# Kernel tuning notes

Hardware: AMD Instinct MI355X
Metric: run time of the kernel (lower is better)

## Reference

```python
import jax, jax.numpy as jnp
import numpy as np

B, S, D, H = 4, 2048, 768, 12
DK = D // H

def setup_inputs() -> dict:
    key = jax.random.key(0)
    ks = jax.random.split(key, 9)
    s = 0.02
    return {
        "z": jax.random.normal(ks[0], (B, S, D), dtype=jnp.float32),
        "wq_w": jax.random.normal(ks[1], (D, D), dtype=jnp.float32) * s,
        "wq_b": jnp.zeros((D,), dtype=jnp.float32),
        "wk_w": jax.random.normal(ks[2], (D, D), dtype=jnp.float32) * s,
        "wk_b": jnp.zeros((D,), dtype=jnp.float32),
        "wv_w": jax.random.normal(ks[3], (D, D), dtype=jnp.float32) * s,
        "wv_b": jnp.zeros((D,), dtype=jnp.float32),
        "fc_w": jax.random.normal(ks[4], (D, D), dtype=jnp.float32) * s,
        "fc_b": jnp.zeros((D,), dtype=jnp.float32),
    }

def reference(z, wq_w, wq_b, wk_w, wk_b, wv_w, wv_b, fc_w, fc_b):
    # Dropout layers are treated as eval-mode (identity), as is standard for
    # a deterministic correctness baseline.
    b, s, d = z.shape
    temp = jnp.asarray(DK ** 0.5, dtype=z.dtype)
    # QKV projections -> [b, h, s, dk]
    def proj(w, bias):
        return (z @ w.T + bias).reshape(b, s, H, DK).transpose(0, 2, 1, 3)
    q = proj(wq_w, wq_b)
    k = proj(wk_w, wk_b)
    v = proj(wv_w, wv_b)
    # raw attention weights (pre-softmax), as returned by ScaleDotAttention
    attn_weights = jnp.einsum('bhqd,bhkd->bhqk', q / temp, k)  # [b,h,s,s]
    attn_probs = jax.nn.softmax(attn_weights, axis=-1)
    context = jnp.einsum('bhqk,bhkd->bhqd', attn_probs, v)  # [b,h,s,dk]
    avg_weights = jnp.sum(attn_weights, axis=1) / H  # [b,s,s]
    context = context.transpose(0, 2, 1, 3).reshape(b, s, d)
    attn_output = context @ fc_w.T + fc_b
    return attn_output, avg_weights
```

## Files before the change

### kernel.cpp

```cpp
#include <hip/hip_runtime.h>
#include <hip/hip_fp16.h>

#define Bc 4
#define Sc 2048
#define Dc 768
#define Hc 12
#define DKc 64

typedef _Float16 f16;
typedef __attribute__((ext_vector_type(8))) _Float16 f16x8;
typedef __attribute__((ext_vector_type(4))) _Float16 f16x4;
typedef __attribute__((ext_vector_type(4))) float f32x4;

static __device__ __forceinline__ f32x4 mfma16(f16x8 a, f16x8 b, f32x4 c) {
  return __builtin_amdgcn_mfma_f32_16x16x32_f16(a, b, c, 0, 0, 0);
}
static __device__ __forceinline__ f32x4 mfma16k16(f16x4 a, f16x4 b, f32x4 c) {
  return __builtin_amdgcn_mfma_f32_16x16x16f16(a, b, c, 0, 0, 0);
}

#define GLD16(g, l)                                              \
  __builtin_amdgcn_global_load_lds(                              \
      (const __attribute__((address_space(1))) void*)(g),        \
      (__attribute__((address_space(3))) void*)(l), 16, 0, 0)

#define SWZ(row, colB) (((row) << 7) + ((colB) ^ (((row) & 7) << 4)))

__global__ __launch_bounds__(256) void cvt5(
    const float* __restrict__ z, const float* __restrict__ w0,
    const float* __restrict__ w1, const float* __restrict__ w2,
    const float* __restrict__ w3, f16* __restrict__ oz, f16* __restrict__ o0,
    f16* __restrict__ o1, f16* __restrict__ o2, f16* __restrict__ o3) {
  const int bid = blockIdx.x;
  const float* in;
  f16* out;
  int i0;
  if (bid < 6144)      { in = z;  out = oz; i0 = bid * 256; }
  else if (bid < 6720) { in = w0; out = o0; i0 = (bid - 6144) * 256; }
  else if (bid < 7296) { in = w1; out = o1; i0 = (bid - 6720) * 256; }
  else if (bid < 7872) { in = w2; out = o2; i0 = (bid - 7296) * 256; }
  else                 { in = w3; out = o3; i0 = (bid - 7872) * 256; }
  const int i = i0 + threadIdx.x;
  float4 v = reinterpret_cast<const float4*>(in)[i];
  f16x4 o;
  o[0] = (f16)v.x; o[1] = (f16)v.y; o[2] = (f16)v.z; o[3] = (f16)v.w;
  reinterpret_cast<f16x4*>(out)[i] = o;
}

template <int MODE>
__global__ __launch_bounds__(512, 2) void gemm128x256(
    const f16* __restrict__ A0, const f16* __restrict__ W0,
    const f16* __restrict__ W1, const f16* __restrict__ W2,
    const float* __restrict__ bq, const float* __restrict__ bk,
    const float* __restrict__ bv, f16* __restrict__ Qb, f16* __restrict__ Kb,
    f16* __restrict__ Vt, float* __restrict__ avg) {
  constexpr int K = Dc;
  constexpr int NK = K / 32;
  const int tid = threadIdx.x;
  const int lane = tid & 63;
  const int w = tid >> 6;
  const int wr = w >> 2, wc = w & 3;
  const int l15 = lane & 15, lg = lane >> 4;

  const f16* Ab;
  const f16* Bb;
  long m0;
  int seg = 0, n0seg = 0, bat = 0, ncol0 = 0;
  if (MODE == 0) {
    const int wgid = (blockIdx.x & 7) * 72 + (blockIdx.x >> 3);
    const int mx = wgid / 9, nt = wgid % 9;
    m0 = (long)mx * 128;
    seg = nt / 3;
    n0seg = (nt % 3) * 256;
    const f16* Wsel = seg == 0 ? W0 : seg == 1 ? W1 : W2;
    Ab = A0 + m0 * K;
    Bb = Wsel + (long)n0seg * K;
  } else if (MODE == 1) {
    const int wgid = (blockIdx.x & 7) * 64 + (blockIdx.x >> 3);
    bat = wgid >> 7;
    const int t = wgid & 127;
    const int mx = t >> 3, nx = t & 7;
    m0 = (long)mx * 128;
    ncol0 = nx * 256;
    Ab = W0 + (long)bat * Sc * Dc + m0 * K;
    Bb = W1 + (long)bat * Sc * Dc + (long)ncol0 * K;
  } else {
    const int wgid = (blockIdx.x & 7) * 24 + (blockIdx.x >> 3);
    const int mx = wgid / 3, nx = wgid % 3;
    m0 = (long)mx * 128;
    ncol0 = nx * 256;
    Ab = A0 + m0 * K;
    Bb = W0 + (long)ncol0 * K;
  }

  __shared__ f16 As[2][128 * 32];
  __shared__ f16 Bs[2][256 * 32];

  const int lr = lane >> 2;
  const int lc = (lane & 3) * 8;
  const f16* Ag0 = Ab + (long)(w * 16 + lr) * K + lc;
  const f16* Bg0 = Bb + (long)(w * 32 + lr) * K + lc;
  const f16* Bg1 = Bg0 + (long)16 * K;

#define STG(buf, k0)                            \
  {                                             \
    GLD16(Ag0 + (k0), &As[buf][w * 512]);       \
    GLD16(Bg0 + (k0), &Bs[buf][w * 1024]);      \
    GLD16(Bg1 + (k0), &Bs[buf][w * 1024 + 512]);\
  }

  f32x4 acc[4][4] = {};

  STG(0, 0)
  STG(1, 32)

#pragma unroll 1
  for (int i = 0; i < NK; ++i) {
    if (i + 1 < NK) {
      asm volatile("s_waitcnt vmcnt(3)" ::: "memory");
    } else {
      asm volatile("s_waitcnt vmcnt(0)" ::: "memory");
    }
    __builtin_amdgcn_sched_barrier(0);
    __builtin_amdgcn_s_barrier();
    __builtin_amdgcn_sched_barrier(0);

    const f16* Asb = &As[i & 1][0];
    const f16* Bsb = &Bs[i & 1][0];
    f16x8 af[4], bf[4];
#pragma unroll
    for (int mi = 0; mi < 4; ++mi)
      af[mi] = *reinterpret_cast<const f16x8*>(
          &Asb[(wr * 64 + mi * 16 + l15) * 32 + lg * 8]);
#pragma unroll
    for (int ni = 0; ni < 4; ++ni)
      bf[ni] = *reinterpret_cast<const f16x8*>(
          &Bsb[(wc * 64 + ni * 16 + l15) * 32 + lg * 8]);
#pragma unroll
    for (int mi = 0; mi < 4; ++mi)
#pragma unroll
      for (int ni = 0; ni < 4; ++ni)
        acc[mi][ni] = mfma16(af[mi], bf[ni], acc[mi][ni]);

    __builtin_amdgcn_sched_barrier(0);
    __builtin_amdgcn_s_barrier();
    __builtin_amdgcn_sched_barrier(0);
    if (i + 2 < NK) STG(i & 1, (i + 2) * 32)
  }
#undef STG

  if (MODE == 0) {
    const float* bias = seg == 0 ? bq : seg == 1 ? bk : bv;
    float bvv[4];
#pragma unroll
    for (int ni = 0; ni < 4; ++ni)
      bvv[ni] = bias[n0seg + wc * 64 + ni * 16 + l15];
    if (seg < 2) {
      f16* dq = seg == 0 ? Qb : Kb;
#pragma unroll
      for (int mi = 0; mi < 4; ++mi) {
#pragma unroll
        for (int ni = 0; ni < 4; ++ni) {
          const long col = n0seg + wc * 64 + ni * 16 + l15;
#pragma unroll
          for (int j = 0; j < 4; ++j) {
            const long row = m0 + wr * 64 + mi * 16 + lg * 4 + j;
            dq[row * Dc + col] = (f16)(acc[mi][ni][j] + bvv[ni]);
          }
        }
      }
    } else {
#pragma unroll
      for (int mi = 0; mi < 4; ++mi) {
#pragma unroll
        for (int ni = 0; ni < 4; ++ni) {
          const long col = n0seg + wc * 64 + ni * 16 + l15;
#pragma unroll
          for (int j = 0; j < 4; ++j) {
            const long row = m0 + wr * 64 + mi * 16 + lg * 4 + j;
            const long b = row >> 11, s = row & 2047;
            Vt[(b * Dc + col) * (long)Sc + s] = (f16)(acc[mi][ni][j] + bvv[ni]);
          }
        }
      }
    }
  } else if (MODE == 1) {
    float* dp = avg + (long)bat * Sc * Sc;
#pragma unroll
    for (int mi = 0; mi < 4; ++mi) {
#pragma unroll
      for (int ni = 0; ni < 4; ++ni) {
        const long col = ncol0 + wc * 64 + ni * 16 + l15;
#pragma unroll
        for (int j = 0; j < 4; ++j) {
          const long row = m0 + wr * 64 + mi * 16 + lg * 4 + j;
          dp[row * Sc + col] = acc[mi][ni][j] * (1.0f / 96.0f);
        }
      }
    }
  } else {
#pragma unroll
    for (int mi = 0; mi < 4; ++mi) {
#pragma unroll
      for (int ni = 0; ni < 4; ++ni) {
        const long col = ncol0 + wc * 64 + ni * 16 + l15;
        const float bv = bq[col];
#pragma unroll
        for (int j = 0; j < 4; ++j) {
          const long row = m0 + wr * 64 + mi * 16 + lg * 4 + j;
          avg[row * Dc + col] = acc[mi][ni][j] + bv;
        }
      }
    }
  }
}

__global__ __launch_bounds__(512) void attn8(const f16* __restrict__ Q,
                                             const f16* __restrict__ Km,
                                             const f16* __restrict__ Vt,
                                             f16* __restrict__ ctx) {
  const int tid = threadIdx.x;
  const int lane = tid & 63;
  const int w = tid >> 6;
  const int l15 = lane & 15, lg = lane >> 4;
  const int lid = (blockIdx.x & 7) * 96 + (blockIdx.x >> 3);
  const int qt = lid & 15;
  const int h  = (lid >> 4) % Hc;
  const int b  = lid / (16 * Hc);
  const int q0 = qt * 128 + w * 16;

  __shared__ f16 Ks[2][64 * 64];
  __shared__ f16 Vs[2][64 * 64];

  f16x8 qf[2];
  {
    const f16* qp = Q + ((long)(b * Sc + q0 + l15)) * Dc + h * DKc + lg * 8;
    qf[0] = *reinterpret_cast<const f16x8*>(qp);
    qf[1] = *reinterpret_cast<const f16x8*>(qp + 32);
  }

  const int srow = tid >> 3;
  const int scolB = (tid & 7) * 16;
  const f16* Kg = Km + (long)(b * Sc) * Dc + h * DKc;
  const f16* Vg = Vt + ((long)(b * Dc + h * DKc)) * Sc;

  const float c2 = 0.18033688011f;
  float m2 = -1e30f, l_run = 0.f;
  f32x4 o[4] = {};

  *reinterpret_cast<f16x8*>((char*)Ks[0] + SWZ(srow, scolB)) =
      *reinterpret_cast<const f16x8*>(Kg + (long)srow * Dc + scolB / 2);
  *reinterpret_cast<f16x8*>((char*)Vs[0] + SWZ(srow, scolB)) =
      *reinterpret_cast<const f16x8*>(Vg + (long)srow * Sc + scolB / 2);
  __syncthreads();

#pragma unroll 1
  for (int i = 0; i < Sc / 64; ++i) {
    const int kv0 = i * 64;
    const bool pf = (i + 1) < Sc / 64;
    char* kb = (char*)Ks[i & 1];
    char* vb = (char*)Vs[i & 1];
    f16x8 kr, vr;
    if (pf) {
      kr = *reinterpret_cast<const f16x8*>(Kg + (long)(kv0 + 64 + srow) * Dc + scolB / 2);
      vr = *reinterpret_cast<const f16x8*>(Vg + (long)srow * Sc + kv0 + 64 + scolB / 2);
    }

    f32x4 sc[4];
    __builtin_amdgcn_s_setprio(1);
#pragma unroll
    for (int t = 0; t < 4; ++t) {
      const int row = t * 16 + l15;
      f32x4 s = {};
      s = mfma16(*reinterpret_cast<const f16x8*>(kb + SWZ(row, lg * 16)), qf[0], s);
      s = mfma16(*reinterpret_cast<const f16x8*>(kb + SWZ(row, 64 + lg * 16)), qf[1], s);
      sc[t] = s;
    }
    __builtin_amdgcn_s_setprio(0);

    float mx = sc[0][0];
#pragma unroll
    for (int t = 0; t < 4; ++t)
#pragma unroll
      for (int j = 0; j < 4; ++j) mx = fmaxf(mx, sc[t][j]);
    const float mx2 = mx * c2;
    float al = 1.0f;
    if (!__all(mx2 <= m2 + 11.544f)) {
      float g = fmaxf(mx2, __shfl_xor(mx2, 16));
      g = fmaxf(g, __shfl_xor(g, 32));
      const float mn2 = fmaxf(m2, g);
      al = __builtin_amdgcn_exp2f(m2 - mn2);
      m2 = mn2;
#pragma unroll
      for (int c = 0; c < 4; ++c)
#pragma unroll
        for (int j = 0; j < 4; ++j) o[c][j] *= al;
    }
    float ps = 0.f;
    f16x4 pp[4];
#pragma unroll
    for (int t = 0; t < 4; ++t)
#pragma unroll
      for (int j = 0; j < 4; ++j) {
        float p = __builtin_amdgcn_exp2f(__builtin_fmaf(sc[t][j], c2, -m2));
        pp[t][j] = (f16)p;
        ps += p;
      }
    ps += __shfl_xor(ps, 16);
    ps += __shfl_xor(ps, 32);
    l_run = l_run * al + ps;

    __builtin_amdgcn_s_setprio(1);
#pragma unroll
    for (int c = 0; c < 4; ++c) {
      const int row = c * 16 + l15;
      f32x4 oc = o[c];
#pragma unroll
      for (int t = 0; t < 4; ++t) {
        f16x4 va = *reinterpret_cast<const f16x4*>(vb + SWZ(row, t * 32 + lg * 8));
        oc = mfma16k16(va, pp[t], oc);
      }
      o[c] = oc;
    }
    __builtin_amdgcn_s_setprio(0);

    if (pf) {
      *reinterpret_cast<f16x8*>((char*)Ks[(i + 1) & 1] + SWZ(srow, scolB)) = kr;
      *reinterpret_cast<f16x8*>((char*)Vs[(i + 1) & 1] + SWZ(srow, scolB)) = vr;
      __syncthreads();
    }
  }

  const float inv = 1.0f / l_run;
  f16* cp = ctx + ((long)(b * Sc) + q0 + l15) * Dc + h * DKc;
#pragma unroll
  for (int c = 0; c < 4; ++c) {
    f16x4 ov;
#pragma unroll
    for (int j = 0; j < 4; ++j) ov[j] = (f16)(o[c][j] * inv);
    *reinterpret_cast<f16x4*>(cp + c * 16 + lg * 4) = ov;
  }
}

extern "C" void kernel_launch(void* const* d_in, const int* in_sizes, int n_in,
                              void* d_out, int out_size, void* d_ws, size_t ws_size,
                              hipStream_t stream) {
  (void)in_sizes; (void)n_in; (void)out_size; (void)ws_size;
  const float* z    = (const float*)d_in[0];
  const float* wq_w = (const float*)d_in[1];
  const float* wq_b = (const float*)d_in[2];
  const float* wk_w = (const float*)d_in[3];
  const float* wk_b = (const float*)d_in[4];
  const float* wv_w = (const float*)d_in[5];
  const float* wv_b = (const float*)d_in[6];
  const float* fc_w = (const float*)d_in[7];
  const float* fc_b = (const float*)d_in[8];
  float* out = (float*)d_out;

  char* ws = (char*)d_ws;
  size_t off = 0;
  auto alloc = [&](size_t bytes) -> void* {
    void* p = (void*)(ws + off);
    off += (bytes + 255) & ~(size_t)255;
    return p;
  };
  const size_t zdb = (size_t)Bc * Sc * Dc * sizeof(f16);
  const size_t wdb = (size_t)Dc * Dc * sizeof(f16);
  f16* zb  = (f16*)alloc(zdb);
  f16* wqb = (f16*)alloc(wdb);
  f16* wkb = (f16*)alloc(wdb);
  f16* wvb = (f16*)alloc(wdb);
  f16* fcb = (f16*)alloc(wdb);
  f16* Qb  = (f16*)alloc(zdb);
  f16* Kb  = (f16*)alloc(zdb);
  f16* Vt  = (f16*)alloc(zdb);
  f16* Cx  = zb;

  cvt5<<<8448, 256, 0, stream>>>(z, wq_w, wk_w, wv_w, fc_w, zb, wqb, wkb, wvb, fcb);

  gemm128x256<0><<<576, 512, 0, stream>>>(zb, wqb, wkb, wvb, wq_b, wk_b, wv_b,
                                          Qb, Kb, Vt, nullptr);

  gemm128x256<1><<<512, 512, 0, stream>>>(nullptr, Qb, Kb, nullptr, nullptr,
                                          nullptr, nullptr, nullptr, nullptr,
                                          nullptr, out + (size_t)Bc * Sc * Dc);

  attn8<<<Bc * Hc * (Sc / 128), 512, 0, stream>>>(Qb, Kb, Vt, Cx);

  gemm128x256<2><<<192, 512, 0, stream>>>(Cx, fcb, nullptr, nullptr, fc_b,
                                          nullptr, nullptr, nullptr, nullptr,
                                          nullptr, out);
}
```

Before: 229.8 us.

## Software-pipeline QK^T one tile ahead of softmax and PV in attention kernel

Restructures the attention loop so the QK^T MFMAs for tile i are issued before the softmax and PV work for tile i-1, which lets the matrix engine overlap the exp/max VALU work. P is staged through a per-wave LDS buffer so PV can use 16x16x32 MFMAs instead of 16x16x16. Row sums now use packed fdot2 and the max uses a max3 tree. It adds an LDS round trip and a second barrier per iteration, and it raises register pressure from keeping two score tiles live.

After: 211.7 us. 1.09x faster.

```diff
diff --git a/kernel.cpp b/kernel.cpp
--- a/kernel.cpp
+++ b/kernel.cpp
@@ -10,14 +10,17 @@
 typedef _Float16 f16;
 typedef __attribute__((ext_vector_type(8))) _Float16 f16x8;
 typedef __attribute__((ext_vector_type(4))) _Float16 f16x4;
+typedef __attribute__((ext_vector_type(2))) _Float16 f16x2;
+typedef __attribute__((ext_vector_type(2))) __fp16 h2raw;
 typedef __attribute__((ext_vector_type(4))) float f32x4;
 
 static __device__ __forceinline__ f32x4 mfma16(f16x8 a, f16x8 b, f32x4 c) {
   return __builtin_amdgcn_mfma_f32_16x16x32_f16(a, b, c, 0, 0, 0);
 }
-static __device__ __forceinline__ f32x4 mfma16k16(f16x4 a, f16x4 b, f32x4 c) {
-  return __builtin_amdgcn_mfma_f32_16x16x16f16(a, b, c, 0, 0, 0);
-}
+static __device__ __forceinline__ float fdot2f(h2raw a, h2raw b, float c) {
+  return __builtin_amdgcn_fdot2(a, b, c, false);
+}
+#define M3(a, b, c) fmaxf(fmaxf((a), (b)), (c))
 
 #define GLD16(g, l)                                              \
   __builtin_amdgcn_global_load_lds(                              \
@@ -231,6 +234,8 @@
 
   __shared__ f16 Ks[2][64 * 64];
   __shared__ f16 Vs[2][64 * 64];
+  __shared__ f16 Ps[8 * 16 * 64];
+  char* pb = (char*)Ps + (w << 11);
 
   f16x8 qf[2];
   {
@@ -238,6 +243,8 @@
     qf[0] = *reinterpret_cast<const f16x8*>(qp);
     qf[1] = *reinterpret_cast<const f16x8*>(qp + 32);
   }
+  h2raw one2;
+  one2[0] = (__fp16)1.0f; one2[1] = (__fp16)1.0f;
 
   const int srow = tid >> 3;
   const int scolB = (tid & 7) * 16;
@@ -248,87 +255,122 @@
   float m2 = -1e30f, l_run = 0.f;
   f32x4 o[4] = {};
 
+#define SMAX_PV(SC, VB)                                                        \
+  {                                                                            \
+    const float t0 = M3(SC[0][0], SC[0][1], SC[0][2]);                         \
+    const float t1 = M3(SC[0][3], SC[1][0], SC[1][1]);                         \
+    const float t2 = M3(SC[1][2], SC[1][3], SC[2][0]);                         \
+    const float t3 = M3(SC[2][1], SC[2][2], SC[2][3]);                         \
+    const float t4 = M3(SC[3][0], SC[3][1], SC[3][2]);                         \
+    float mx = M3(t0, t1, t2);                                                 \
+    mx = M3(mx, t3, t4);                                                       \
+    mx = fmaxf(mx, SC[3][3]);                                                  \
+    const float mx2 = mx * c2;                                                 \
+    float al = 1.0f;                                                           \
+    if (!__all(mx2 <= m2 + 11.544f)) {                                         \
+      float g = fmaxf(mx2, __shfl_xor(mx2, 16));                               \
+      g = fmaxf(g, __shfl_xor(g, 32));                                         \
+      const float mn2 = fmaxf(m2, g);                                          \
+      al = __builtin_amdgcn_exp2f(m2 - mn2);                                   \
+      m2 = mn2;                                                                \
+      _Pragma("unroll") for (int c = 0; c < 4; ++c)                            \
+        _Pragma("unroll") for (int j = 0; j < 4; ++j) o[c][j] *= al;           \
+    }                                                                          \
+    float ps = 0.f;                                                            \
+    f16x4 pp[4];                                                               \
+    _Pragma("unroll") for (int t = 0; t < 4; ++t) {                            \
+      const float p0 = __builtin_amdgcn_exp2f(__builtin_fmaf(SC[t][0], c2, -m2)); \
+      const float p1 = __builtin_amdgcn_exp2f(__builtin_fmaf(SC[t][1], c2, -m2)); \
+      const float p2 = __builtin_amdgcn_exp2f(__builtin_fmaf(SC[t][2], c2, -m2)); \
+      const float p3 = __builtin_amdgcn_exp2f(__builtin_fmaf(SC[t][3], c2, -m2)); \
+      const h2raw lo = __builtin_amdgcn_cvt_pkrtz(p0, p1);                     \
+      const h2raw hi = __builtin_amdgcn_cvt_pkrtz(p2, p3);                     \
+      const f16x2 lo2 = __builtin_bit_cast(f16x2, lo);                         \
+      const f16x2 hi2 = __builtin_bit_cast(f16x2, hi);                         \
+      pp[t][0] = lo2[0]; pp[t][1] = lo2[1]; pp[t][2] = hi2[0]; pp[t][3] = hi2[1]; \
+      ps = fdot2f(lo, one2, ps);                                               \
+      ps = fdot2f(hi, one2, ps);                                               \
+    }                                                                          \
+    ps += __shfl_xor(ps, 16);                                                  \
+    ps += __shfl_xor(ps, 32);                                                  \
+    l_run = l_run * al + ps;                                                   \
+    _Pragma("unroll") for (int t = 0; t < 4; ++t)                              \
+      *reinterpret_cast<f16x4*>(pb + SWZ(l15, t * 32 + lg * 8)) = pp[t];       \
+    asm volatile("s_waitcnt lgkmcnt(0)" ::: "memory");                         \
+    __builtin_amdgcn_sched_barrier(0);                                         \
+    f16x8 pa0 = *reinterpret_cast<const f16x8*>(pb + SWZ(l15, lg * 16));       \
+    f16x8 pa1 = *reinterpret_cast<const f16x8*>(pb + SWZ(l15, 64 + lg * 16));  \
+    __builtin_amdgcn_s_setprio(1);                                             \
+    _Pragma("unroll") for (int c = 0; c < 4; ++c) {                            \
+      const int row = c * 16 + l15;                                            \
+      o[c] = mfma16(*reinterpret_cast<const f16x8*>((VB) + SWZ(row, lg * 16)), pa0, o[c]); \
+      o[c] = mfma16(*reinterpret_cast<const f16x8*>((VB) + SWZ(row, 64 + lg * 16)), pa1, o[c]); \
+    }                                                                          \
+    __builtin_amdgcn_s_setprio(0);                                             \
+  }
+
   *reinterpret_cast<f16x8*>((char*)Ks[0] + SWZ(srow, scolB)) =
       *reinterpret_cast<const f16x8*>(Kg + (long)srow * Dc + scolB / 2);
   *reinterpret_cast<f16x8*>((char*)Vs[0] + SWZ(srow, scolB)) =
       *reinterpret_cast<const f16x8*>(Vg + (long)srow * Sc + scolB / 2);
+  *reinterpret_cast<f16x8*>((char*)Ks[1] + SWZ(srow, scolB)) =
+      *reinterpret_cast<const f16x8*>(Kg + (long)(64 + srow) * Dc + scolB / 2);
+  *reinterpret_cast<f16x8*>((char*)Vs[1] + SWZ(srow, scolB)) =
+      *reinterpret_cast<const f16x8*>(Vg + (long)srow * Sc + 64 + scolB / 2);
   __syncthreads();
 
-#pragma unroll 1
-  for (int i = 0; i < Sc / 64; ++i) {
-    const int kv0 = i * 64;
-    const bool pf = (i + 1) < Sc / 64;
-    char* kb = (char*)Ks[i & 1];
-    char* vb = (char*)Vs[i & 1];
-    f16x8 kr, vr;
-    if (pf) {
-      kr = *reinterpret_cast<const f16x8*>(Kg + (long)(kv0 + 64 + srow) * Dc + scolB / 2);
-      vr = *reinterpret_cast<const f16x8*>(Vg + (long)srow * Sc + kv0 + 64 + scolB / 2);
-    }
-
-    f32x4 sc[4];
-    __builtin_amdgcn_s_setprio(1);
+  f32x4 scp[4];
+  {
+    char* kb = (char*)Ks[0];
 #pragma unroll
     for (int t = 0; t < 4; ++t) {
       const int row = t * 16 + l15;
       f32x4 s = {};
       s = mfma16(*reinterpret_cast<const f16x8*>(kb + SWZ(row, lg * 16)), qf[0], s);
       s = mfma16(*reinterpret_cast<const f16x8*>(kb + SWZ(row, 64 + lg * 16)), qf[1], s);
-      sc[t] = s;
-    }
-    __builtin_amdgcn_s_setprio(0);
-
-    float mx = sc[0][0];
-#pragma unroll
-    for (int t = 0; t < 4; ++t)
-#pragma unroll
-      for (int j = 0; j < 4; ++j) mx = fmaxf(mx, sc[t][j]);
-    const float mx2 = mx * c2;
-    float al = 1.0f;
-    if (!__all(mx2 <= m2 + 11.544f)) {
-      float g = fmaxf(mx2, __shfl_xor(mx2, 16));
-      g = fmaxf(g, __shfl_xor(g, 32));
-      const float mn2 = fmaxf(m2, g);
-      al = __builtin_amdgcn_exp2f(m2 - mn2);
-      m2 = mn2;
-#pragma unroll
-      for (int c = 0; c < 4; ++c)
-#pragma unroll
-        for (int j = 0; j < 4; ++j) o[c][j] *= al;
-    }
-    float ps = 0.f;
-    f16x4 pp[4];
-#pragma unroll
-    for (int t = 0; t < 4; ++t)
-#pragma unroll
-      for (int j = 0; j < 4; ++j) {
-        float p = __builtin_amdgcn_exp2f(__builtin_fmaf(sc[t][j], c2, -m2));
-        pp[t][j] = (f16)p;
-        ps += p;
+      scp[t] = s;
+    }
+  }
+
+#pragma unroll 1
+  for (int i = 1; i < Sc / 64; ++i) {
+    const bool pf = (i + 1) < Sc / 64;
+    f16x8 kr, vr;
+    if (pf) {
+      kr = *reinterpret_cast<const f16x8*>(Kg + (long)((i + 1) * 64 + srow) * Dc + scolB / 2);
+      vr = *reinterpret_cast<const f16x8*>(Vg + (long)srow * Sc + (i + 1) * 64 + scolB / 2);
+    }
+
+    f32x4 scc[4];
+    {
+      char* kb = (char*)Ks[i & 1];
+#pragma unroll
+      for (int t = 0; t < 4; ++t) {
+        const int row = t * 16 + l15;
+        f32x4 s = {};
+        s = mfma16(*reinterpret_cast<const f16x8*>(kb + SWZ(row, lg * 16)), qf[0], s);
+        s = mfma16(*reinterpret_cast<const f16x8*>(kb + SWZ(row, 64 + lg * 16)), qf[1], s);
+        scc[t] = s;
       }
-    ps += __shfl_xor(ps, 16);
-    ps += __shfl_xor(ps, 32);
-    l_run = l_run * al + ps;
-
-    __builtin_amdgcn_s_setprio(1);
-#pragma unroll
-    for (int c = 0; c < 4; ++c) {
-      const int row = c * 16 + l15;
-      f32x4 oc = o[c];
-#pragma unroll
-      for (int t = 0; t < 4; ++t) {
-        f16x4 va = *reinterpret_cast<const f16x4*>(vb + SWZ(row, t * 32 + lg * 8));
-        oc = mfma16k16(va, pp[t], oc);
-      }
-      o[c] = oc;
-    }
-    __builtin_amdgcn_s_setprio(0);
-
+    }
+
+    char* vb = (char*)Vs[(i - 1) & 1];
+    SMAX_PV(scp, vb)
+
+    __syncthreads();
     if (pf) {
       *reinterpret_cast<f16x8*>((char*)Ks[(i + 1) & 1] + SWZ(srow, scolB)) = kr;
       *reinterpret_cast<f16x8*>((char*)Vs[(i + 1) & 1] + SWZ(srow, scolB)) = vr;
-      __syncthreads();
-    }
+    }
+    __syncthreads();
+
+#pragma unroll
+    for (int t = 0; t < 4; ++t) scp[t] = scc[t];
+  }
+
+  {
+    char* vb = (char*)Vs[(Sc / 64 - 1) & 1];
+    SMAX_PV(scp, vb)
   }
 
   const float inv = 1.0f / l_run;
@@ -340,6 +382,7 @@
     for (int j = 0; j < 4; ++j) ov[j] = (f16)(o[c][j] * inv);
     *reinterpret_cast<f16x4*>(cp + c * 16 + lg * 4) = ov;
   }
+#undef SMAX_PV
 }
 
 extern "C" void kernel_launch(void* const* d_in, const int* in_sizes, int n_in,
```
